# Kernel optimization log

Hardware: AMD Instinct MI355X
Metric: run time of the kernel (lower is better)

Reference implementation:

```python
import jax, jax.numpy as jnp
import numpy as np

E = 8      # num experts
K = 2      # top-k
D = 1024   # hidden size
F = 4096   # intermediate size
B, S = 4, 1024


def setup_inputs() -> dict:
    key = jax.random.key(0)
    ks = jax.random.split(key, 5)
    s = 0.02
    return {
        "hidden_states": jax.random.normal(ks[0], (B, S, D), jnp.float32),
        "gate_w": jax.random.normal(ks[1], (D, E), jnp.float32) * s,   # Linear, no bias
        "fc_w": jax.random.normal(ks[2], (E, D, F), jnp.float32) * s,  # Conv1D weight [in,out]
        "fc_b": jnp.zeros((E, F), jnp.float32),
        "proj_w": jax.random.normal(ks[3], (E, F, D), jnp.float32) * s,
        "proj_b": jnp.zeros((E, D), jnp.float32),
    }


def reference(hidden_states, gate_w, fc_w, fc_b, proj_w, proj_b):
    b, s, d = hidden_states.shape
    x = hidden_states.reshape(-1, d)                       # [T, D]
    router_logits = x @ gate_w                             # [T, E]
    probs = jax.nn.softmax(router_logits.astype(jnp.float32), axis=-1)
    routing_weights, selected_experts = jax.lax.top_k(probs, K)   # [T, K]
    routing_weights = routing_weights / routing_weights.sum(-1, keepdims=True)
    routing_weights = routing_weights.astype(x.dtype)

    out = jnp.zeros_like(x)
    # Fixed small loop over experts (structurally distinct weights).
    # Dense mask-weighted compute == gather/MLP/scatter-add of the original
    # (tokens not routed to expert e get weight 0).
    for e in range(E):
        w_e = jnp.sum(routing_weights * (selected_experts == e), axis=-1)  # [T]
        h = jax.nn.gelu(x @ fc_w[e] + fc_b[e], approximate=True)           # gelu_new
        h = h @ proj_w[e] + proj_b[e]
        out = out + h * w_e[:, None]

    return out.reshape(b, s, d), router_logits
```

## Files before the change

### kernel.cpp

```cpp
#include <hip/hip_runtime.h>
#include <hip/hip_bf16.h>


#define T_TOK 4096
#define D_DIM 1024
#define F_DIM 4096
#define E_NUM 8
#define CAP   9216

typedef short short8 __attribute__((ext_vector_type(8)));
typedef float f32x4  __attribute__((ext_vector_type(4)));

__device__ __forceinline__ void async_ld16(const void* g, void* l) {
  __builtin_amdgcn_global_load_lds(
      (const __attribute__((address_space(1))) char*)g,
      (__attribute__((address_space(3))) char*)l,
      16, 0, 0);
}

__global__ void transpose_cast(const float* __restrict__ in, __hip_bfloat16* __restrict__ out,
                               int R, int C) {
  __shared__ float t[64][65];
  const int ex = blockIdx.z;
  in  += (size_t)ex * R * C;
  out += (size_t)ex * R * C;
  const int r0 = blockIdx.y * 64, c0 = blockIdx.x * 64;
  const int tx = threadIdx.x & 15;
  const int ty = threadIdx.x >> 4;
#pragma unroll
  for (int i = 0; i < 4; ++i) {
    const int r = ty + i * 16;
    const float4 v = *(const float4*)(in + (size_t)(r0 + r) * C + c0 + tx * 4);
    t[r][tx * 4 + 0] = v.x; t[r][tx * 4 + 1] = v.y;
    t[r][tx * 4 + 2] = v.z; t[r][tx * 4 + 3] = v.w;
  }
  __syncthreads();
#pragma unroll
  for (int i = 0; i < 4; ++i) {
    const int c = ty + i * 16;
    union { __hip_bfloat16 h[4]; ushort4 u; } pk;
#pragma unroll
    for (int k = 0; k < 4; ++k) pk.h[k] = __float2bfloat16(t[tx * 4 + k][c]);
    *(ushort4*)(out + (size_t)(c0 + c) * R + r0 + tx * 4) = pk.u;
  }
}

__global__ void router_kernel(const float* __restrict__ x, const float* __restrict__ gw,
                              float* __restrict__ logits, int* __restrict__ counts,
                              int* __restrict__ tk_e, int* __restrict__ tk_pos,
                              float* __restrict__ tk_w) {
  const int lane = threadIdx.x & 63;
  const int t = blockIdx.x * 4 + (threadIdx.x >> 6);
  const float* xr = x + (size_t)t * D_DIM;
  float a[8] = {0.f, 0.f, 0.f, 0.f, 0.f, 0.f, 0.f, 0.f};
  for (int it = 0; it < D_DIM / 64; ++it) {
    const int d = lane + it * 64;
    const float xv = xr[d];
    const float4 g0 = *(const float4*)(gw + d * 8);
    const float4 g1 = *(const float4*)(gw + d * 8 + 4);
    a[0] += xv * g0.x; a[1] += xv * g0.y; a[2] += xv * g0.z; a[3] += xv * g0.w;
    a[4] += xv * g1.x; a[5] += xv * g1.y; a[6] += xv * g1.z; a[7] += xv * g1.w;
  }
#pragma unroll
  for (int off = 32; off > 0; off >>= 1)
#pragma unroll
    for (int e = 0; e < 8; ++e) a[e] += __shfl_down(a[e], off);
  if (lane == 0) {
    float mx = a[0];
#pragma unroll
    for (int e = 1; e < 8; ++e) mx = fmaxf(mx, a[e]);
    float p[8];
#pragma unroll
    for (int e = 0; e < 8; ++e) p[e] = __expf(a[e] - mx);
    int i1 = 0;
#pragma unroll
    for (int e = 1; e < 8; ++e) if (p[e] > p[i1]) i1 = e;
    int i2 = (i1 == 0) ? 1 : 0;
#pragma unroll
    for (int e = 0; e < 8; ++e) if (e != i1 && p[e] > p[i2]) i2 = e;
    const float inv = 1.f / (p[i1] + p[i2]);
#pragma unroll
    for (int e = 0; e < 8; ++e) logits[(size_t)t * 8 + e] = a[e];
    const int p1 = atomicAdd(counts + i1, 1);
    const int p2 = atomicAdd(counts + i2, 1);
    tk_e[t * 2]     = i1; tk_pos[t * 2]     = p1; tk_w[t * 2]     = p[i1] * inv;
    tk_e[t * 2 + 1] = i2; tk_pos[t * 2 + 1] = p2; tk_w[t * 2 + 1] = p[i2] * inv;
  }
}

__global__ void prefix_kernel(const int* __restrict__ counts, int* __restrict__ bases) {
  if (threadIdx.x == 0 && blockIdx.x == 0) {
    int b = 0;
    for (int e = 0; e < 8; ++e) { bases[e] = b; b += (counts[e] + 127) & ~127; }
    bases[8] = b;
  }
}

__global__ void gather_kernel(const float* __restrict__ x, const int* __restrict__ bases,
                              const int* __restrict__ tk_e, const int* __restrict__ tk_pos,
                              const float* __restrict__ tk_w,
                              __hip_bfloat16* __restrict__ Xg,
                              int* __restrict__ slot_token, float* __restrict__ slot_weight) {
  const int b = blockIdx.x;
  const int t = b >> 1;
  const int slot = bases[tk_e[b]] + tk_pos[b];
  if (threadIdx.x == 0) { slot_token[slot] = t; slot_weight[slot] = tk_w[b]; }
  const float4 v = ((const float4*)(x + (size_t)t * D_DIM))[threadIdx.x];
  union { __hip_bfloat16 h[4]; ushort4 u; } pk;
  pk.h[0] = __float2bfloat16(v.x);
  pk.h[1] = __float2bfloat16(v.y);
  pk.h[2] = __float2bfloat16(v.z);
  pk.h[3] = __float2bfloat16(v.w);
  ((ushort4*)(Xg + (size_t)slot * D_DIM))[threadIdx.x] = pk.u;
}

template <int N, int K, int KSPLIT, bool IS_FC>
__global__ __launch_bounds__(256, 2) void moe_gemm(
    const __hip_bfloat16* __restrict__ A, const __hip_bfloat16* __restrict__ Bt,
    const float* __restrict__ bias, const int* __restrict__ counts,
    const int* __restrict__ bases, __hip_bfloat16* __restrict__ Hout,
    const int* __restrict__ slot_token, const float* __restrict__ slot_weight,
    float* __restrict__ out) {
  __shared__ __align__(16) __hip_bfloat16 As[128 * 32];
  __shared__ __align__(16) __hip_bfloat16 Bs[128 * 32];

  const int m0 = blockIdx.y * 128;
  const int total = bases[8];
  if (m0 >= total) return;
  int e = 0;
#pragma unroll
  for (int i = 1; i < 8; ++i) e = (m0 >= bases[i]) ? i : e;
  const int n0 = blockIdx.x * 128;
  constexpr int KC = K / KSPLIT;
  const int kbase = blockIdx.z * KC;

  const __hip_bfloat16* Ab = A + (size_t)m0 * K + kbase;
  const __hip_bfloat16* Bb = Bt + ((size_t)e * N + n0) * K + kbase;

  const int tid = threadIdx.x;
  const int lane = tid & 63;
  const int wave = tid >> 6;
  const int wm = (wave >> 1) * 64;
  const int wn = (wave & 1) * 64;
  const int lr = lane & 15;
  const int quad = lane >> 4;

  f32x4 acc[4][4] = {};

  const int c0 = tid, c1 = tid + 256;
  const int ar0 = c0 >> 2, ac0 = (c0 & 3) * 8;
  const int ar1 = c1 >> 2, ac1 = (c1 & 3) * 8;

  for (int k0 = 0; k0 < KC; k0 += 32) {
    async_ld16(Ab + (size_t)ar0 * K + k0 + ac0, As + c0 * 8);
    async_ld16(Ab + (size_t)ar1 * K + k0 + ac1, As + c1 * 8);
    async_ld16(Bb + (size_t)ar0 * K + k0 + ac0, Bs + c0 * 8);
    async_ld16(Bb + (size_t)ar1 * K + k0 + ac1, Bs + c1 * 8);
    __syncthreads();

    short8 af[4], bfr[4];
#pragma unroll
    for (int i = 0; i < 4; ++i)
      af[i] = *(const short8*)(As + (wm + i * 16 + lr) * 32 + quad * 8);
#pragma unroll
    for (int j = 0; j < 4; ++j)
      bfr[j] = *(const short8*)(Bs + (wn + j * 16 + lr) * 32 + quad * 8);
#pragma unroll
    for (int i = 0; i < 4; ++i)
#pragma unroll
      for (int j = 0; j < 4; ++j)
        acc[i][j] = __builtin_amdgcn_mfma_f32_16x16x32_bf16(af[i], bfr[j], acc[i][j], 0, 0, 0);
    __syncthreads();
  }

  if (IS_FC) {
#pragma unroll
    for (int j = 0; j < 4; ++j) {
      const int nc = n0 + wn + j * 16 + lr;
      const float bv = bias[(size_t)e * N + nc];
#pragma unroll
      for (int i = 0; i < 4; ++i) {
#pragma unroll
        for (int r = 0; r < 4; ++r) {
          const int row = m0 + wm + i * 16 + quad * 4 + r;
          const float v = acc[i][j][r] + bv;
          const float u2 = 1.5957691216057308f * (v + 0.044715f * v * v * v);
          const float g = v / (1.0f + __expf(-u2));
          Hout[(size_t)row * N + nc] = __float2bfloat16(g);
        }
      }
    }
  } else {
    const int base_e = bases[e];
    const int cnt = counts[e];
    const float bscale = (blockIdx.z == 0) ? 1.0f : 0.0f;
#pragma unroll
    for (int i = 0; i < 4; ++i) {
#pragma unroll
      for (int r = 0; r < 4; ++r) {
        const int row = m0 + wm + i * 16 + quad * 4 + r;
        if (row - base_e < cnt) {
          const float w = slot_weight[row];
          const int t = slot_token[row];
          float* orow = out + (size_t)t * D_DIM;
#pragma unroll
          for (int j = 0; j < 4; ++j) {
            const int nc = n0 + wn + j * 16 + lr;
            atomicAdd(orow + nc, (acc[i][j][r] + bscale * bias[(size_t)e * N + nc]) * w);
          }
        }
      }
    }
  }
}

extern "C" void kernel_launch(void* const* d_in, const int* in_sizes, int n_in,
                              void* d_out, int out_size, void* d_ws, size_t ws_size,
                              hipStream_t stream) {
  const float* x      = (const float*)d_in[0];
  const float* gate_w = (const float*)d_in[1];
  const float* fc_w   = (const float*)d_in[2];
  const float* fc_b   = (const float*)d_in[3];
  const float* proj_w = (const float*)d_in[4];
  const float* proj_b = (const float*)d_in[5];
  float* out = (float*)d_out;
  float* logits = out + (size_t)T_TOK * D_DIM;

  char* ws = (char*)d_ws;
  __hip_bfloat16* fcT   = (__hip_bfloat16*)(ws);
  __hip_bfloat16* projT = (__hip_bfloat16*)(ws + 67108864LL);
  __hip_bfloat16* Xg    = (__hip_bfloat16*)(ws + 134217728LL);
  __hip_bfloat16* Hg    = (__hip_bfloat16*)(ws + 153092096LL);
  int* meta = (int*)(ws + 228589568LL);
  int*   counts      = meta;
  int*   bases       = meta + 8;
  int*   tk_e        = meta + 20;
  int*   tk_pos      = tk_e + 8192;
  float* tk_w        = (float*)(tk_pos + 8192);
  int*   slot_token  = (int*)(tk_w + 8192);
  float* slot_weight = (float*)(slot_token + CAP);

  hipMemsetAsync(d_out, 0, (size_t)out_size * sizeof(float), stream);
  hipMemsetAsync(counts, 0, 8 * sizeof(int), stream);

  transpose_cast<<<dim3(F_DIM / 64, D_DIM / 64, E_NUM), 256, 0, stream>>>(fc_w, fcT, D_DIM, F_DIM);
  transpose_cast<<<dim3(D_DIM / 64, F_DIM / 64, E_NUM), 256, 0, stream>>>(proj_w, projT, F_DIM, D_DIM);

  router_kernel<<<T_TOK / 4, 256, 0, stream>>>(x, gate_w, logits, counts, tk_e, tk_pos, tk_w);
  prefix_kernel<<<1, 64, 0, stream>>>(counts, bases);
  gather_kernel<<<T_TOK * 2, 256, 0, stream>>>(x, bases, tk_e, tk_pos, tk_w, Xg,
                                               slot_token, slot_weight);

  moe_gemm<F_DIM, D_DIM, 1, true><<<dim3(F_DIM / 128, CAP / 128, 1), 256, 0, stream>>>(
      Xg, fcT, fc_b, counts, bases, Hg, nullptr, nullptr, nullptr);
  moe_gemm<D_DIM, F_DIM, 4, false><<<dim3(D_DIM / 128, CAP / 128, 4), 256, 0, stream>>>(
      Hg, projT, proj_b, counts, bases, nullptr, slot_token, slot_weight, out);
}
```

Measured before the change: 757.4 us.

## Replace split-K atomic scatter with per-slot partial buffer and combine kernel

The proj GEMM no longer splits K across four blocks with float atomicAdd into the output. It now uses a 128x64 tile over the full K and writes weighted per-slot rows into a float buffer that reuses the fcT workspace region, and a new combine kernel sums each token's two slots. This drops the output memset, the slot_token array and all atomic contention, at the cost of a buffer write/read and an extra launch. The narrower N tile keeps the proj grid large without split-K but gives each block less reuse.

New measurement: 696.0 us. 1.09x faster.

```diff
diff --git a/kernel.cpp b/kernel.cpp
--- a/kernel.cpp
+++ b/kernel.cpp
@@ -100,11 +100,11 @@
                               const int* __restrict__ tk_e, const int* __restrict__ tk_pos,
                               const float* __restrict__ tk_w,
                               __hip_bfloat16* __restrict__ Xg,
-                              int* __restrict__ slot_token, float* __restrict__ slot_weight) {
+                              float* __restrict__ slot_weight) {
   const int b = blockIdx.x;
   const int t = b >> 1;
   const int slot = bases[tk_e[b]] + tk_pos[b];
-  if (threadIdx.x == 0) { slot_token[slot] = t; slot_weight[slot] = tk_w[b]; }
+  if (threadIdx.x == 0) slot_weight[slot] = tk_w[b];
   const float4 v = ((const float4*)(x + (size_t)t * D_DIM))[threadIdx.x];
   union { __hip_bfloat16 h[4]; ushort4 u; } pk;
   pk.h[0] = __float2bfloat16(v.x);
@@ -114,68 +114,79 @@
   ((ushort4*)(Xg + (size_t)slot * D_DIM))[threadIdx.x] = pk.u;
 }
 
-template <int N, int K, int KSPLIT, bool IS_FC>
+__global__ void combine_kernel(const float* __restrict__ P, const int* __restrict__ bases,
+                               const int* __restrict__ tk_e, const int* __restrict__ tk_pos,
+                               float* __restrict__ out) {
+  const int t = blockIdx.x;
+  const int s1 = bases[tk_e[2 * t]]     + tk_pos[2 * t];
+  const int s2 = bases[tk_e[2 * t + 1]] + tk_pos[2 * t + 1];
+  const int d = threadIdx.x * 4;
+  const float4 a = *(const float4*)(P + (size_t)s1 * D_DIM + d);
+  const float4 b = *(const float4*)(P + (size_t)s2 * D_DIM + d);
+  float4 o; o.x = a.x + b.x; o.y = a.y + b.y; o.z = a.z + b.z; o.w = a.w + b.w;
+  *(float4*)(out + (size_t)t * D_DIM + d) = o;
+}
+
+template <int N, int K, int BN, bool IS_FC>
 __global__ __launch_bounds__(256, 2) void moe_gemm(
     const __hip_bfloat16* __restrict__ A, const __hip_bfloat16* __restrict__ Bt,
     const float* __restrict__ bias, const int* __restrict__ counts,
     const int* __restrict__ bases, __hip_bfloat16* __restrict__ Hout,
-    const int* __restrict__ slot_token, const float* __restrict__ slot_weight,
-    float* __restrict__ out) {
+    const float* __restrict__ slot_weight, float* __restrict__ Pout) {
   __shared__ __align__(16) __hip_bfloat16 As[128 * 32];
-  __shared__ __align__(16) __hip_bfloat16 Bs[128 * 32];
+  __shared__ __align__(16) __hip_bfloat16 Bs[BN * 32];
 
   const int m0 = blockIdx.y * 128;
-  const int total = bases[8];
-  if (m0 >= total) return;
+  if (m0 >= bases[8]) return;
   int e = 0;
 #pragma unroll
   for (int i = 1; i < 8; ++i) e = (m0 >= bases[i]) ? i : e;
-  const int n0 = blockIdx.x * 128;
-  constexpr int KC = K / KSPLIT;
-  const int kbase = blockIdx.z * KC;
-
-  const __hip_bfloat16* Ab = A + (size_t)m0 * K + kbase;
-  const __hip_bfloat16* Bb = Bt + ((size_t)e * N + n0) * K + kbase;
+  const int n0 = blockIdx.x * BN;
+
+  const __hip_bfloat16* Ab = A + (size_t)m0 * K;
+  const __hip_bfloat16* Bb = Bt + ((size_t)e * N + n0) * K;
 
   const int tid = threadIdx.x;
   const int lane = tid & 63;
   const int wave = tid >> 6;
   const int wm = (wave >> 1) * 64;
-  const int wn = (wave & 1) * 64;
+  const int wn = (wave & 1) * (BN / 2);
+  constexpr int MJ = BN / 32;
   const int lr = lane & 15;
   const int quad = lane >> 4;
 
-  f32x4 acc[4][4] = {};
+  f32x4 acc[4][MJ] = {};
 
   const int c0 = tid, c1 = tid + 256;
   const int ar0 = c0 >> 2, ac0 = (c0 & 3) * 8;
   const int ar1 = c1 >> 2, ac1 = (c1 & 3) * 8;
 
-  for (int k0 = 0; k0 < KC; k0 += 32) {
+  for (int k0 = 0; k0 < K; k0 += 32) {
     async_ld16(Ab + (size_t)ar0 * K + k0 + ac0, As + c0 * 8);
     async_ld16(Ab + (size_t)ar1 * K + k0 + ac1, As + c1 * 8);
     async_ld16(Bb + (size_t)ar0 * K + k0 + ac0, Bs + c0 * 8);
-    async_ld16(Bb + (size_t)ar1 * K + k0 + ac1, Bs + c1 * 8);
+    if constexpr (BN == 128)
+      async_ld16(Bb + (size_t)ar1 * K + k0 + ac1, Bs + c1 * 8);
     __syncthreads();
 
-    short8 af[4], bfr[4];
+    short8 af[4], bfr[MJ];
 #pragma unroll
     for (int i = 0; i < 4; ++i)
       af[i] = *(const short8*)(As + (wm + i * 16 + lr) * 32 + quad * 8);
 #pragma unroll
-    for (int j = 0; j < 4; ++j)
+    for (int j = 0; j < MJ; ++j)
       bfr[j] = *(const short8*)(Bs + (wn + j * 16 + lr) * 32 + quad * 8);
 #pragma unroll
     for (int i = 0; i < 4; ++i)
 #pragma unroll
-      for (int j = 0; j < 4; ++j)
+      for (int j = 0; j < MJ; ++j)
         acc[i][j] = __builtin_amdgcn_mfma_f32_16x16x32_bf16(af[i], bfr[j], acc[i][j], 0, 0, 0);
     __syncthreads();
   }
 
   if (IS_FC) {
 #pragma unroll
-    for (int j = 0; j < 4; ++j) {
+    for (int j = 0; j < MJ; ++j) {
       const int nc = n0 + wn + j * 16 + lr;
       const float bv = bias[(size_t)e * N + nc];
 #pragma unroll
@@ -193,7 +204,6 @@
   } else {
     const int base_e = bases[e];
     const int cnt = counts[e];
-    const float bscale = (blockIdx.z == 0) ? 1.0f : 0.0f;
 #pragma unroll
     for (int i = 0; i < 4; ++i) {
 #pragma unroll
@@ -201,12 +211,10 @@
         const int row = m0 + wm + i * 16 + quad * 4 + r;
         if (row - base_e < cnt) {
           const float w = slot_weight[row];
-          const int t = slot_token[row];
-          float* orow = out + (size_t)t * D_DIM;
-#pragma unroll
-          for (int j = 0; j < 4; ++j) {
+#pragma unroll
+          for (int j = 0; j < MJ; ++j) {
             const int nc = n0 + wn + j * 16 + lr;
-            atomicAdd(orow + nc, (acc[i][j][r] + bscale * bias[(size_t)e * N + nc]) * w);
+            Pout[(size_t)row * N + nc] = (acc[i][j][r] + bias[(size_t)e * N + nc]) * w;
           }
         }
       }
@@ -228,6 +236,7 @@
 
   char* ws = (char*)d_ws;
   __hip_bfloat16* fcT   = (__hip_bfloat16*)(ws);
+  float*          P     = (float*)(ws);
   __hip_bfloat16* projT = (__hip_bfloat16*)(ws + 67108864LL);
   __hip_bfloat16* Xg    = (__hip_bfloat16*)(ws + 134217728LL);
   __hip_bfloat16* Hg    = (__hip_bfloat16*)(ws + 153092096LL);
@@ -237,10 +246,8 @@
   int*   tk_e        = meta + 20;
   int*   tk_pos      = tk_e + 8192;
   float* tk_w        = (float*)(tk_pos + 8192);
-  int*   slot_token  = (int*)(tk_w + 8192);
-  float* slot_weight = (float*)(slot_token + CAP);
-
-  hipMemsetAsync(d_out, 0, (size_t)out_size * sizeof(float), stream);
+  float* slot_weight = (float*)(tk_w + 8192);
+
   hipMemsetAsync(counts, 0, 8 * sizeof(int), stream);
 
   transpose_cast<<<dim3(F_DIM / 64, D_DIM / 64, E_NUM), 256, 0, stream>>>(fc_w, fcT, D_DIM, F_DIM);
@@ -248,11 +255,11 @@
 
   router_kernel<<<T_TOK / 4, 256, 0, stream>>>(x, gate_w, logits, counts, tk_e, tk_pos, tk_w);
   prefix_kernel<<<1, 64, 0, stream>>>(counts, bases);
-  gather_kernel<<<T_TOK * 2, 256, 0, stream>>>(x, bases, tk_e, tk_pos, tk_w, Xg,
-                                               slot_token, slot_weight);
-
-  moe_gemm<F_DIM, D_DIM, 1, true><<<dim3(F_DIM / 128, CAP / 128, 1), 256, 0, stream>>>(
-      Xg, fcT, fc_b, counts, bases, Hg, nullptr, nullptr, nullptr);
-  moe_gemm<D_DIM, F_DIM, 4, false><<<dim3(D_DIM / 128, CAP / 128, 4), 256, 0, stream>>>(
-      Hg, projT, proj_b, counts, bases, nullptr, slot_token, slot_weight, out);
-}
+  gather_kernel<<<T_TOK * 2, 256, 0, stream>>>(x, bases, tk_e, tk_pos, tk_w, Xg, slot_weight);
+
+  moe_gemm<F_DIM, D_DIM, 128, true><<<dim3(F_DIM / 128, CAP / 128), 256, 0, stream>>>(
+      Xg, fcT, fc_b, counts, bases, Hg, nullptr, nullptr);
+  moe_gemm<D_DIM, F_DIM, 64, false><<<dim3(D_DIM / 64, CAP / 128), 256, 0, stream>>>(
+      Hg, projT, proj_b, counts, bases, nullptr, slot_weight, P);
+  combine_kernel<<<T_TOK, 256, 0, stream>>>(P, bases, tk_e, tk_pos, out);
+}
```
